# Optimization experiments

Hardware: AMD Instinct MI355X
Metric: run time of the kernel (lower is better)

Reference implementation:

```python
import jax, jax.numpy as jnp
import numpy as np

N = 50000
E = 800000
F_IN = 256
HEADS = 4
C = 64
NEG_SLOPE = 0.2


def setup_inputs() -> dict:
    key = jax.random.key(0)
    ks = jax.random.split(key, 7)
    x = jax.random.normal(ks[0], (N, F_IN), dtype=jnp.float32)
    edge_index = jax.random.randint(ks[1], (2, E), 0, N, dtype=jnp.int64)
    # Glorot-ish scaling for weights
    W = jax.random.normal(ks[2], (F_IN, HEADS * C), dtype=jnp.float32) / np.sqrt(F_IN)
    att_src = jax.random.normal(ks[3], (HEADS, C), dtype=jnp.float32) / np.sqrt(C)
    att_dst = jax.random.normal(ks[4], (HEADS, C), dtype=jnp.float32) / np.sqrt(C)
    bias = jnp.zeros((HEADS * C,), dtype=jnp.float32)
    prelu_a = jnp.full((1,), 0.25, dtype=jnp.float32)  # PReLU default init
    return {"x": x, "edge_index": edge_index, "W": W, "att_src": att_src,
            "att_dst": att_dst, "bias": bias, "prelu_a": prelu_a}


def _gat_forward(x, edge_index, W, att_src, att_dst, bias, prelu_a):
    n = x.shape[0]
    # add self loops (PyG GATConv default)
    loops = jnp.arange(n, dtype=edge_index.dtype)
    src = jnp.concatenate([edge_index[0], loops])  # message source j
    dst = jnp.concatenate([edge_index[1], loops])  # message target i

    h = (x @ W).reshape(n, HEADS, C)                    # [N,H,C]
    a_src = jnp.einsum('nhc,hc->nh', h, att_src)        # [N,H]
    a_dst = jnp.einsum('nhc,hc->nh', h, att_dst)        # [N,H]

    e = a_src[src] + a_dst[dst]                         # [Etot,H]
    e = jnp.where(e >= 0, e, NEG_SLOPE * e)             # LeakyReLU(0.2)

    # numerically stable softmax over edges grouped by destination node
    m = jax.ops.segment_max(e, dst, num_segments=n)     # [N,H]
    alpha = jnp.exp(e - m[dst])
    denom = jax.ops.segment_sum(alpha, dst, num_segments=n)
    alpha = alpha / (denom[dst] + 1e-16)                # [Etot,H]

    msg = alpha[:, :, None] * h[src]                    # [Etot,H,C]
    out = jax.ops.segment_sum(msg, dst, num_segments=n) # [N,H,C]
    out = out.reshape(n, HEADS * C) + bias
    # PReLU with single shared parameter
    return jnp.where(out >= 0, out, prelu_a * out)


def reference(x, edge_index, W, att_src, att_dst, bias, prelu_a):
    return _gat_forward(x, edge_index, W, att_src, att_dst, bias, prelu_a)
```

## Files before the change

kernel.cpp:

```cpp
#include <hip/hip_runtime.h>
#include <stdint.h>


using u16 = unsigned short;
typedef float f32x4 __attribute__((ext_vector_type(4)));
typedef __bf16 bf16x8 __attribute__((ext_vector_type(8)));
typedef u16 u16x8 __attribute__((ext_vector_type(8)));

#define NEG 0.2f
#define APAD 264
#define NBLK1 256

__device__ __forceinline__ float bf2f(u16 u) {
    union { uint32_t i; float f; } v; v.i = ((uint32_t)u) << 16; return v.f;
}
__device__ __forceinline__ u16 f2bf(float f) {
    union { float f; uint32_t i; } v; v.f = f;
    uint32_t r = v.i + 0x7FFFu + ((v.i >> 16) & 1u);
    return (u16)(r >> 16);
}
__device__ __forceinline__ void split2(float f, u16& h, u16& l) {
    union { float f; uint32_t i; } v; v.f = f;
    h = (u16)(v.i >> 16);
    float r = f - bf2f(h);
    union { float f; uint32_t i; } w; w.f = r;
    l = (u16)(w.i >> 16);
}
__device__ __forceinline__ float wexp(float e) {
    e = e >= 0.f ? e : NEG * e;
    return __expf(e);
}

__global__ __launch_bounds__(256) void prep_kernel(
    const float* __restrict__ W, u16* __restrict__ Wfh, u16* __restrict__ Wfl,
    unsigned* __restrict__ bflag, int nscan)
{
    const int tid = threadIdx.x;
    const int gt = blockIdx.x * 256 + tid;
    if (gt < nscan) bflag[gt] = 0u;
    const int f = blockIdx.x * 4 + (tid >> 6);
    const int l = tid & 63;
    const int kg = f >> 4, nb = f & 15;
    const int n = nb * 16 + (l & 15);
    const int kb = kg * 32 + (l >> 4) * 8;
    u16x8 hv, lv;
#pragma unroll
    for (int j = 0; j < 8; j++) {
        u16 th, tl;
        split2(W[(size_t)(kb + j) * 256 + n], th, tl);
        hv[j] = th;
        lv[j] = tl;
    }
    *(u16x8*)(Wfh + ((size_t)f * 64 + l) * 8) = hv;
    *(u16x8*)(Wfl + ((size_t)f * 64 + l) * 8) = lv;
}

__global__ __launch_bounds__(256, 2) void gemm_kernel(
    const float* __restrict__ X, const u16* __restrict__ Wfh,
    const u16* __restrict__ Wfl, const float* __restrict__ attS,
    const float* __restrict__ attD, u16* __restrict__ H,
    float* __restrict__ a_src, float* __restrict__ a_dst, int Nn)
{
    __shared__ u16 Ah[64 * APAD];
    __shared__ u16 Al[64 * APAD];
    const int tid = threadIdx.x, m0 = blockIdx.x * 64;
    const int wave = tid >> 6, lane = tid & 63;
    const int quad = lane >> 4, lr = lane & 15;

#pragma unroll
    for (int i = 0; i < 16; i++) {
        const int f = i * 256 + tid;
        const int row = f >> 6;
        const int c4 = (f & 63) * 4;
        int grow = m0 + row;
        if (grow >= Nn) grow = Nn - 1;
        const float4 v = *(const float4*)(X + (size_t)grow * 256 + c4);
        u16 h0, l0, h1, l1, h2, l2, h3, l3;
        split2(v.x, h0, l0); split2(v.y, h1, l1);
        split2(v.z, h2, l2); split2(v.w, h3, l3);
        uint2 hp, lp;
        hp.x = (uint32_t)h0 | ((uint32_t)h1 << 16);
        hp.y = (uint32_t)h2 | ((uint32_t)h3 << 16);
        lp.x = (uint32_t)l0 | ((uint32_t)l1 << 16);
        lp.y = (uint32_t)l2 | ((uint32_t)l3 << 16);
        *(uint2*)(Ah + row * APAD + c4) = hp;
        *(uint2*)(Al + row * APAD + c4) = lp;
    }
    __syncthreads();

    f32x4 acc[4][4] = {};
    bf16x8 bh[2][4], bl[2][4];

#pragma unroll
    for (int ni = 0; ni < 4; ni++) {
        const size_t o = ((size_t)(wave * 4 + ni) * 64 + lane) * 8;
        bh[0][ni] = *(const bf16x8*)(Wfh + o);
        bl[0][ni] = *(const bf16x8*)(Wfl + o);
    }

#pragma unroll
    for (int kg = 0; kg < 8; kg++) {
        const int st = kg & 1, ns = st ^ 1;
        if (kg < 7) {
#pragma unroll
            for (int ni = 0; ni < 4; ni++) {
                const size_t o = ((size_t)((kg + 1) * 16 + wave * 4 + ni) * 64 + lane) * 8;
                bh[ns][ni] = *(const bf16x8*)(Wfh + o);
                bl[ns][ni] = *(const bf16x8*)(Wfl + o);
            }
        }
        bf16x8 ah[4], al[4];
#pragma unroll
        for (int mi = 0; mi < 4; mi++) {
            const int o = (mi * 16 + lr) * APAD + kg * 32 + quad * 8;
            ah[mi] = *(const bf16x8*)(Ah + o);
            al[mi] = *(const bf16x8*)(Al + o);
        }
#pragma unroll
        for (int ni = 0; ni < 4; ni++)
#pragma unroll
            for (int mi = 0; mi < 4; mi++) {
                acc[mi][ni] = __builtin_amdgcn_mfma_f32_16x16x32_bf16(
                    ah[mi], bh[st][ni], acc[mi][ni], 0, 0, 0);
                acc[mi][ni] = __builtin_amdgcn_mfma_f32_16x16x32_bf16(
                    ah[mi], bl[st][ni], acc[mi][ni], 0, 0, 0);
                acc[mi][ni] = __builtin_amdgcn_mfma_f32_16x16x32_bf16(
                    al[mi], bh[st][ni], acc[mi][ni], 0, 0, 0);
            }
    }

    {
        float asv[4], adv[4];
#pragma unroll
        for (int ni = 0; ni < 4; ni++) {
            asv[ni] = attS[wave * 64 + ni * 16 + lr];
            adv[ni] = attD[wave * 64 + ni * 16 + lr];
        }
#pragma unroll
        for (int mi = 0; mi < 4; mi++)
#pragma unroll
            for (int r = 0; r < 4; r++) {
                float ps = 0.f, pd = 0.f;
#pragma unroll
                for (int ni = 0; ni < 4; ni++) {
                    ps += acc[mi][ni][r] * asv[ni];
                    pd += acc[mi][ni][r] * adv[ni];
                }
#pragma unroll
                for (int off = 8; off >= 1; off >>= 1) {
                    ps += __shfl_xor(ps, off, 16);
                    pd += __shfl_xor(pd, off, 16);
                }
                if (lr == 0) {
                    const int row = m0 + mi * 16 + quad * 4 + r;
                    if (row < Nn) {
                        a_src[row * 4 + wave] = ps;
                        a_dst[row * 4 + wave] = pd;
                    }
                }
            }
    }

    const int n0 = wave * 64;
#pragma unroll
    for (int mi = 0; mi < 4; mi++)
#pragma unroll
        for (int ni = 0; ni < 4; ni++) {
            int col = n0 + ni * 16 + lr;
#pragma unroll
            for (int r = 0; r < 4; r++) {
                int row = m0 + mi * 16 + quad * 4 + r;
                if (row < Nn) H[(size_t)row * 256 + col] = f2bf(acc[mi][ni][r]);
            }
        }
}

__global__ __launch_bounds__(256) void p1hist_kernel(
    const int* __restrict__ edst, int* __restrict__ cnt1,
    int E, int Nn, int nb1, int chunk)
{
    __shared__ int h1[256];
    const int tid = threadIdx.x;
    h1[tid] = 0;
    __syncthreads();
    const int e0 = blockIdx.x * chunk;
    const int e1 = (e0 + chunk < E) ? e0 + chunk : E;
    for (int e = e0 + tid; e < e1; e += 256) {
        int i = edst[e];
        i = ((unsigned)i < (unsigned)Nn) ? i : 0;
        atomicAdd(&h1[i >> 8], 1);
    }
    __syncthreads();
    if (tid < nb1) cnt1[tid * NBLK1 + blockIdx.x] = h1[tid];
}

#define SCAN_READY 0x80000000u
__global__ __launch_bounds__(1024) void scan_kernel(
    const int* __restrict__ in, int* __restrict__ out,
    unsigned* __restrict__ bflag, int len)
{
    __shared__ int wsum[16];
    __shared__ int sprefix;
    const int t = threadIdx.x, wv = t >> 6, ln = t & 63;
    const int b = blockIdx.x;
    const int idx = b * 1024 + t;
    int v = (idx < len) ? in[idx] : 0;
    int s = v;
#pragma unroll
    for (int o = 1; o < 64; o <<= 1) {
        int u = __shfl_up(s, o, 64);
        if (ln >= o) s += u;
    }
    if (ln == 63) wsum[wv] = s;
    __syncthreads();
    if (t == 0) {
        int run = 0;
#pragma unroll
        for (int w = 0; w < 16; w++) { int x = wsum[w]; wsum[w] = run; run += x; }
        atomicExch(&bflag[b], (unsigned)run | SCAN_READY);
        unsigned pre = 0;
        for (int pb = b - 1; pb >= 0; pb--) {
            unsigned f;
            do { f = atomicAdd(&bflag[pb], 0u); } while (!(f & SCAN_READY));
            pre += f & ~SCAN_READY;
        }
        sprefix = (int)pre;
    }
    __syncthreads();
    if (idx < len) out[idx] = sprefix + wsum[wv] + s - v;
}

__global__ __launch_bounds__(256) void p1scat_kernel(
    const int* __restrict__ esrc, const int* __restrict__ edst,
    const int* __restrict__ base1, uint32_t* __restrict__ part,
    int E, int Nn, int nb1, int chunk)
{
    __shared__ int cur1[256];
    const int tid = threadIdx.x;
    if (tid < nb1) cur1[tid] = base1[tid * NBLK1 + blockIdx.x];
    __syncthreads();
    const int e0 = blockIdx.x * chunk;
    const int e1 = (e0 + chunk < E) ? e0 + chunk : E;
    for (int e = e0 + tid; e < e1; e += 256) {
        int i = edst[e];
        i = ((unsigned)i < (unsigned)Nn) ? i : 0;
        int j = esrc[e];
        j = ((unsigned)j < (unsigned)Nn) ? j : 0;
        const int pos = atomicAdd(&cur1[i >> 8], 1);
        part[pos] = (uint32_t)j | ((uint32_t)(i & 255) << 16);
    }
}

__global__ __launch_bounds__(256) void p2_kernel(
    const uint32_t* __restrict__ part, const int* __restrict__ base1,
    int* __restrict__ deg, int* __restrict__ offs, int* __restrict__ csr_src,
    int E, int Nn, int nb1)
{
    __shared__ int h2[256];
    __shared__ int wsum[4];
    const int b = blockIdx.x, tid = threadIdx.x;
    const int ln = tid & 63, wv = tid >> 6;
    const int bstart = base1[b * NBLK1];
    const int bend = (b == nb1 - 1) ? E : base1[(b + 1) * NBLK1];
    h2[tid] = 0;
    __syncthreads();
    for (int e = bstart + tid; e < bend; e += 256)
        atomicAdd(&h2[part[e] >> 16], 1);
    __syncthreads();
    const int cnt = h2[tid];
    int s = cnt;
#pragma unroll
    for (int o = 1; o < 64; o <<= 1) {
        int u = __shfl_up(s, o, 64);
        if (ln >= o) s += u;
    }
    if (ln == 63) wsum[wv] = s;
    __syncthreads();
    int wpre = 0;
#pragma unroll
    for (int w2 = 0; w2 < 4; w2++) wpre += (w2 < wv) ? wsum[w2] : 0;
    const int ex = bstart + wpre + s - cnt;
    const int node = (b << 8) + tid;
    if (node < Nn) { deg[node] = cnt; offs[node] = ex; }
    __syncthreads();
    h2[tid] = ex;
    __syncthreads();
    for (int e = bstart + tid; e < bend; e += 256) {
        const uint32_t p = part[e];
        const int pos = atomicAdd(&h2[p >> 16], 1);
        csr_src[pos] = (int)(p & 0xFFFFu);
    }
}

__global__ __launch_bounds__(256) void gather_kernel(
    const u16* __restrict__ H, const int* __restrict__ offs,
    const int* __restrict__ deg, const int* __restrict__ csr_src,
    const float* __restrict__ a_src, const float* __restrict__ a_dst,
    const float* __restrict__ bias, const float* __restrict__ prelu,
    float* __restrict__ out, int Nn)
{
    const int wave = threadIdx.x >> 6, lane = threadIdx.x & 63;
    const int g = blockIdx.x >> 3, s = blockIdx.x & 7;
    const int hp = s >> 2;
    const int node = ((g << 2) + (s & 3)) * 4 + wave;
    if (node >= Nn) return;
    const int hh = lane >> 5;
    const int head = (hp << 1) + hh;
    const int sub = lane & 31;
    const int ch = (head << 6) + sub * 2;

    const float adv = a_dst[node * 4 + head];
    const float ws = wexp(a_src[node * 4 + head] + adv);
    float acc0, acc1, sumw = 0.f;
    {
        const uint32_t hv = *(const uint32_t*)(H + (size_t)node * 256 + ch);
        acc0 = ws * bf2f((u16)hv);
        acc1 = ws * bf2f((u16)(hv >> 16));
    }
    const int d = deg[node];
    const int* __restrict__ cp = csr_src + offs[node];

    for (int k = 0; k < d; k += 32) {
        const int q = d - k;
        const int es = (sub < q) ? sub : q - 1;
        const int jj = cp[k + es];
        float ww = wexp(a_src[jj * 4 + head] + adv);
        ww = (sub < q) ? ww : 0.f;
        sumw += ww;
        const int nh = (q > 16) ? 2 : 1;
        for (int half = 0; half < nh; half++) {
            const int hb = half << 4;
            uint32_t hv[16];
#pragma unroll
            for (int t = 0; t < 16; t++) {
                const int jt = __shfl(jj, hb + t, 32);
                hv[t] = *(const uint32_t*)(H + ((size_t)jt << 8) + ch);
            }
#pragma unroll
            for (int t = 0; t < 16; t++) {
                const float w = __shfl(ww, hb + t, 32);
                acc0 += w * bf2f((u16)hv[t]);
                acc1 += w * bf2f((u16)(hv[t] >> 16));
            }
        }
    }
#pragma unroll
    for (int off = 16; off >= 1; off >>= 1)
        sumw += __shfl_xor(sumw, off, 32);

    const float inv = 1.f / (ws + sumw + 1e-16f);
    const float pa = prelu[0];
    float o0 = acc0 * inv + bias[ch];
    float o1 = acc1 * inv + bias[ch + 1];
    o0 = o0 >= 0.f ? o0 : pa * o0;
    o1 = o1 >= 0.f ? o1 : pa * o1;
    float2 ov; ov.x = o0; ov.y = o1;
    *(float2*)(out + (size_t)node * 256 + ch) = ov;
}

extern "C" void kernel_launch(void* const* d_in, const int* in_sizes, int n_in,
                              void* d_out, int out_size, void* d_ws, size_t ws_size,
                              hipStream_t stream)
{
    const float* X    = (const float*)d_in[0];
    const int*   EI   = (const int*)d_in[1];
    const float* W    = (const float*)d_in[2];
    const float* attS = (const float*)d_in[3];
    const float* attD = (const float*)d_in[4];
    const float* bias = (const float*)d_in[5];
    const float* pa   = (const float*)d_in[6];

    const int Nn = in_sizes[0] / 256;
    const int E  = in_sizes[1] / 2;
    const int* esrc = EI;
    const int* edst = EI + E;

    const int nb1   = (Nn + 255) >> 8;
    const int slen  = nb1 * NBLK1;
    const int nscan = (slen + 1023) / 1024;
    const int chunk = (E + NBLK1 - 1) / NBLK1;

    char* p = (char*)d_ws;
    u16*      H       = (u16*)p;      p += (size_t)Nn * 256 * 2;
    float*    a_src   = (float*)p;    p += (size_t)Nn * 4 * 4;
    float*    a_dst   = (float*)p;    p += (size_t)Nn * 4 * 4;
    u16*      Wfh     = (u16*)p;      p += 256 * 256 * 2;
    u16*      Wfl     = (u16*)p;      p += 256 * 256 * 2;
    int*      deg     = (int*)p;      p += (size_t)Nn * 4;
    int*      offs    = (int*)p;      p += (size_t)Nn * 4;
    int*      cnt1    = (int*)p;      p += (size_t)256 * NBLK1 * 4;
    int*      base1   = (int*)p;      p += (size_t)256 * NBLK1 * 4;
    unsigned* bflag   = (unsigned*)p; p += 256 * 4;
    uint32_t* part    = (uint32_t*)p; p += (size_t)E * 4;
    int*      csr_src = (int*)p;      p += ((size_t)E + 16) * 4;

    prep_kernel<<<32, 256, 0, stream>>>(W, Wfh, Wfl, bflag, nscan);
    gemm_kernel<<<(Nn + 63) / 64, 256, 0, stream>>>(X, Wfh, Wfl, attS, attD,
                                                    H, a_src, a_dst, Nn);
    p1hist_kernel<<<NBLK1, 256, 0, stream>>>(edst, cnt1, E, Nn, nb1, chunk);
    scan_kernel<<<nscan, 1024, 0, stream>>>(cnt1, base1, bflag, slen);
    p1scat_kernel<<<NBLK1, 256, 0, stream>>>(esrc, edst, base1, part,
                                             E, Nn, nb1, chunk);
    p2_kernel<<<nb1, 256, 0, stream>>>(part, base1, deg, offs, csr_src,
                                       E, Nn, nb1);
    const int gblocks = ((Nn + 15) / 16) * 8;
    gather_kernel<<<gblocks, 256, 0, stream>>>(H, offs, deg, csr_src,
                                               a_src, a_dst, bias, pa,
                                               (float*)d_out, Nn);
}
```

Baseline: 240.2 us.

## Fuse CSR build kernels into one persistent kernel with grid barriers

Replaces the four CSR-construction kernels (histogram, decoupled-lookback scan, partition scatter, per-bucket sort) with a single 256-block kernel separated by atomic-counter grid barriers. The scan becomes a two-level per-bucket scan plus a bucket-sum scan. The goal is to remove three kernel launch gaps and the serial lookback chain. It relies on all 256 blocks being co-resident, which holds on a 256-CU device but is not guaranteed, and spin barriers add their own latency.

```diff
diff --git a/kernel.cpp b/kernel.cpp
--- a/kernel.cpp
+++ b/kernel.cpp
@@ -31,13 +31,23 @@
     return __expf(e);
 }
 
+__device__ __forceinline__ void gridbar(unsigned* ctr, unsigned target) {
+    __syncthreads();
+    if (threadIdx.x == 0) {
+        __threadfence();
+        atomicAdd(ctr, 1u);
+        while (atomicAdd(ctr, 0u) < target) __builtin_amdgcn_s_sleep(2);
+        __threadfence();
+    }
+    __syncthreads();
+}
+
 __global__ __launch_bounds__(256) void prep_kernel(
     const float* __restrict__ W, u16* __restrict__ Wfh, u16* __restrict__ Wfl,
-    unsigned* __restrict__ bflag, int nscan)
+    unsigned* __restrict__ ctr)
 {
     const int tid = threadIdx.x;
-    const int gt = blockIdx.x * 256 + tid;
-    if (gt < nscan) bflag[gt] = 0u;
+    if (blockIdx.x == 0 && tid == 0) *ctr = 0u;
     const int f = blockIdx.x * 4 + (tid >> 6);
     const int l = tid & 63;
     const int kg = f >> 4, nb = f & 15;
@@ -53,6 +63,114 @@
     }
     *(u16x8*)(Wfh + ((size_t)f * 64 + l) * 8) = hv;
     *(u16x8*)(Wfl + ((size_t)f * 64 + l) * 8) = lv;
+}
+
+__global__ __launch_bounds__(256) void csrall_kernel(
+    const int* __restrict__ esrc, const int* __restrict__ edst,
+    int* __restrict__ deg, int* __restrict__ offs,
+    int* __restrict__ cnt1, int* __restrict__ base1, int* __restrict__ bsum,
+    unsigned* __restrict__ ctr, uint32_t* __restrict__ part,
+    int* __restrict__ csr_src, int E, int Nn, int nb1, int chunk)
+{
+    __shared__ int lds[256];
+    __shared__ int wsum[4];
+    const int tid = threadIdx.x, cb = blockIdx.x;
+    const int ln = tid & 63, wv = tid >> 6;
+    const int e0 = cb * chunk;
+    const int e1 = (e0 + chunk < E) ? e0 + chunk : E;
+
+    lds[tid] = 0;
+    __syncthreads();
+    for (int e = e0 + tid; e < e1; e += 256) {
+        int i = edst[e];
+        i = ((unsigned)i < (unsigned)Nn) ? i : 0;
+        atomicAdd(&lds[i >> 8], 1);
+    }
+    __syncthreads();
+    if (tid < nb1) cnt1[tid * NBLK1 + cb] = lds[tid];
+    gridbar(ctr, 1u * NBLK1);
+
+    if (cb < nb1) {
+        const int v = cnt1[cb * NBLK1 + tid];
+        int s = v;
+#pragma unroll
+        for (int o = 1; o < 64; o <<= 1) {
+            int u = __shfl_up(s, o, 64);
+            if (ln >= o) s += u;
+        }
+        if (ln == 63) wsum[wv] = s;
+        __syncthreads();
+        int wpre = 0;
+#pragma unroll
+        for (int w2 = 0; w2 < 4; w2++) wpre += (w2 < wv) ? wsum[w2] : 0;
+        base1[cb * NBLK1 + tid] = wpre + s - v;
+        if (tid == 255) bsum[cb] = wpre + s;
+        __syncthreads();
+    }
+    gridbar(ctr, 2u * NBLK1);
+
+    if (cb == 0) {
+        const int v = (tid < nb1) ? bsum[tid] : 0;
+        int s = v;
+#pragma unroll
+        for (int o = 1; o < 64; o <<= 1) {
+            int u = __shfl_up(s, o, 64);
+            if (ln >= o) s += u;
+        }
+        if (ln == 63) wsum[wv] = s;
+        __syncthreads();
+        int wpre = 0;
+#pragma unroll
+        for (int w2 = 0; w2 < 4; w2++) wpre += (w2 < wv) ? wsum[w2] : 0;
+        if (tid < nb1) bsum[tid] = wpre + s - v;
+    }
+    gridbar(ctr, 3u * NBLK1);
+
+    if (tid < nb1) lds[tid] = bsum[tid] + base1[tid * NBLK1 + cb];
+    __syncthreads();
+    for (int e = e0 + tid; e < e1; e += 256) {
+        int i = edst[e];
+        i = ((unsigned)i < (unsigned)Nn) ? i : 0;
+        int j = esrc[e];
+        j = ((unsigned)j < (unsigned)Nn) ? j : 0;
+        const int pos = atomicAdd(&lds[i >> 8], 1);
+        part[pos] = (uint32_t)j | ((uint32_t)(i & 255) << 16);
+    }
+    gridbar(ctr, 4u * NBLK1);
+
+    if (cb < nb1) {
+        const int bstart = bsum[cb];
+        const int bend = (cb + 1 < nb1) ? bsum[cb + 1] : E;
+        lds[tid] = 0;
+        __syncthreads();
+        for (int e = bstart + tid; e < bend; e += 256)
+            atomicAdd(&lds[part[e] >> 16], 1);
+        __syncthreads();
+        const int cnt = lds[tid];
+        int s = cnt;
+#pragma unroll
+        for (int o = 1; o < 64; o <<= 1) {
+            int u = __shfl_up(s, o, 64);
+            if (ln >= o) s += u;
+        }
+        __syncthreads();
+        if (ln == 63) wsum[wv] = s;
+        __syncthreads();
+        int wpre = 0;
+#pragma unroll
+        for (int w2 = 0; w2 < 4; w2++) wpre += (w2 < wv) ? wsum[w2] : 0;
+        const int ex = bstart + wpre + s - cnt;
+        const int node = (cb << 8) + tid;
+        if (node < Nn) { deg[node] = cnt; offs[node] = ex; }
+        __syncthreads();
+        lds[tid] = ex;
+        __syncthreads();
+        for (int e = bstart + tid; e < bend; e += 256) {
+            const uint32_t pr = part[e];
+            const int pos = atomicAdd(&lds[pr >> 16], 1);
+            csr_src[pos] = (int)(pr & 0xFFFFu);
+        }
+    }
 }
 
 __global__ __launch_bounds__(256, 2) void gemm_kernel(
@@ -175,123 +293,6 @@
         }
 }
 
-__global__ __launch_bounds__(256) void p1hist_kernel(
-    const int* __restrict__ edst, int* __restrict__ cnt1,
-    int E, int Nn, int nb1, int chunk)
-{
-    __shared__ int h1[256];
-    const int tid = threadIdx.x;
-    h1[tid] = 0;
-    __syncthreads();
-    const int e0 = blockIdx.x * chunk;
-    const int e1 = (e0 + chunk < E) ? e0 + chunk : E;
-    for (int e = e0 + tid; e < e1; e += 256) {
-        int i = edst[e];
-        i = ((unsigned)i < (unsigned)Nn) ? i : 0;
-        atomicAdd(&h1[i >> 8], 1);
-    }
-    __syncthreads();
-    if (tid < nb1) cnt1[tid * NBLK1 + blockIdx.x] = h1[tid];
-}
-
-#define SCAN_READY 0x80000000u
-__global__ __launch_bounds__(1024) void scan_kernel(
-    const int* __restrict__ in, int* __restrict__ out,
-    unsigned* __restrict__ bflag, int len)
-{
-    __shared__ int wsum[16];
-    __shared__ int sprefix;
-    const int t = threadIdx.x, wv = t >> 6, ln = t & 63;
-    const int b = blockIdx.x;
-    const int idx = b * 1024 + t;
-    int v = (idx < len) ? in[idx] : 0;
-    int s = v;
-#pragma unroll
-    for (int o = 1; o < 64; o <<= 1) {
-        int u = __shfl_up(s, o, 64);
-        if (ln >= o) s += u;
-    }
-    if (ln == 63) wsum[wv] = s;
-    __syncthreads();
-    if (t == 0) {
-        int run = 0;
-#pragma unroll
-        for (int w = 0; w < 16; w++) { int x = wsum[w]; wsum[w] = run; run += x; }
-        atomicExch(&bflag[b], (unsigned)run | SCAN_READY);
-        unsigned pre = 0;
-        for (int pb = b - 1; pb >= 0; pb--) {
-            unsigned f;
-            do { f = atomicAdd(&bflag[pb], 0u); } while (!(f & SCAN_READY));
-            pre += f & ~SCAN_READY;
-        }
-        sprefix = (int)pre;
-    }
-    __syncthreads();
-    if (idx < len) out[idx] = sprefix + wsum[wv] + s - v;
-}
-
-__global__ __launch_bounds__(256) void p1scat_kernel(
-    const int* __restrict__ esrc, const int* __restrict__ edst,
-    const int* __restrict__ base1, uint32_t* __restrict__ part,
-    int E, int Nn, int nb1, int chunk)
-{
-    __shared__ int cur1[256];
-    const int tid = threadIdx.x;
-    if (tid < nb1) cur1[tid] = base1[tid * NBLK1 + blockIdx.x];
-    __syncthreads();
-    const int e0 = blockIdx.x * chunk;
-    const int e1 = (e0 + chunk < E) ? e0 + chunk : E;
-    for (int e = e0 + tid; e < e1; e += 256) {
-        int i = edst[e];
-        i = ((unsigned)i < (unsigned)Nn) ? i : 0;
-        int j = esrc[e];
-        j = ((unsigned)j < (unsigned)Nn) ? j : 0;
-        const int pos = atomicAdd(&cur1[i >> 8], 1);
-        part[pos] = (uint32_t)j | ((uint32_t)(i & 255) << 16);
-    }
-}
-
-__global__ __launch_bounds__(256) void p2_kernel(
-    const uint32_t* __restrict__ part, const int* __restrict__ base1,
-    int* __restrict__ deg, int* __restrict__ offs, int* __restrict__ csr_src,
-    int E, int Nn, int nb1)
-{
-    __shared__ int h2[256];
-    __shared__ int wsum[4];
-    const int b = blockIdx.x, tid = threadIdx.x;
-    const int ln = tid & 63, wv = tid >> 6;
-    const int bstart = base1[b * NBLK1];
-    const int bend = (b == nb1 - 1) ? E : base1[(b + 1) * NBLK1];
-    h2[tid] = 0;
-    __syncthreads();
-    for (int e = bstart + tid; e < bend; e += 256)
-        atomicAdd(&h2[part[e] >> 16], 1);
-    __syncthreads();
-    const int cnt = h2[tid];
-    int s = cnt;
-#pragma unroll
-    for (int o = 1; o < 64; o <<= 1) {
-        int u = __shfl_up(s, o, 64);
-        if (ln >= o) s += u;
-    }
-    if (ln == 63) wsum[wv] = s;
-    __syncthreads();
-    int wpre = 0;
-#pragma unroll
-    for (int w2 = 0; w2 < 4; w2++) wpre += (w2 < wv) ? wsum[w2] : 0;
-    const int ex = bstart + wpre + s - cnt;
-    const int node = (b << 8) + tid;
-    if (node < Nn) { deg[node] = cnt; offs[node] = ex; }
-    __syncthreads();
-    h2[tid] = ex;
-    __syncthreads();
-    for (int e = bstart + tid; e < bend; e += 256) {
-        const uint32_t p = part[e];
-        const int pos = atomicAdd(&h2[p >> 16], 1);
-        csr_src[pos] = (int)(p & 0xFFFFu);
-    }
-}
-
 __global__ __launch_bounds__(256) void gather_kernel(
     const u16* __restrict__ H, const int* __restrict__ offs,
     const int* __restrict__ deg, const int* __restrict__ csr_src,
@@ -376,8 +377,6 @@
     const int* edst = EI + E;
 
     const int nb1   = (Nn + 255) >> 8;
-    const int slen  = nb1 * NBLK1;
-    const int nscan = (slen + 1023) / 1024;
     const int chunk = (E + NBLK1 - 1) / NBLK1;
 
     char* p = (char*)d_ws;
@@ -390,19 +389,17 @@
     int*      offs    = (int*)p;      p += (size_t)Nn * 4;
     int*      cnt1    = (int*)p;      p += (size_t)256 * NBLK1 * 4;
     int*      base1   = (int*)p;      p += (size_t)256 * NBLK1 * 4;
-    unsigned* bflag   = (unsigned*)p; p += 256 * 4;
+    int*      bsum    = (int*)p;      p += 256 * 4;
+    unsigned* ctr     = (unsigned*)p; p += 64 * 4;
     uint32_t* part    = (uint32_t*)p; p += (size_t)E * 4;
     int*      csr_src = (int*)p;      p += ((size_t)E + 16) * 4;
 
-    prep_kernel<<<32, 256, 0, stream>>>(W, Wfh, Wfl, bflag, nscan);
+    prep_kernel<<<32, 256, 0, stream>>>(W, Wfh, Wfl, ctr);
+    csrall_kernel<<<NBLK1, 256, 0, stream>>>(esrc, edst, deg, offs,
+                                             cnt1, base1, bsum, ctr,
+                                             part, csr_src, E, Nn, nb1, chunk);
     gemm_kernel<<<(Nn + 63) / 64, 256, 0, stream>>>(X, Wfh, Wfl, attS, attD,
                                                     H, a_src, a_dst, Nn);
-    p1hist_kernel<<<NBLK1, 256, 0, stream>>>(edst, cnt1, E, Nn, nb1, chunk);
-    scan_kernel<<<nscan, 1024, 0, stream>>>(cnt1, base1, bflag, slen);
-    p1scat_kernel<<<NBLK1, 256, 0, stream>>>(esrc, edst, base1, part,
-                                             E, Nn, nb1, chunk);
-    p2_kernel<<<nb1, 256, 0, stream>>>(part, base1, deg, offs, csr_src,
-                                       E, Nn, nb1);
     const int gblocks = ((Nn + 15) / 16) * 8;
     gather_kernel<<<gblocks, 256, 0, stream>>>(H, offs, deg, csr_src,
                                                a_src, a_dst, bias, pa,
```

New measurement: 312.4 us. 30.1% more time.
